# Performance work log

Hardware: AMD Instinct MI355X
Metric: run time of the kernel (lower is better)

Reference implementation:

```python
import jax, jax.numpy as jnp
import numpy as np


def setup_inputs() -> dict:
    key = jax.random.key(0)
    k1, k2, k3 = jax.random.split(key, 3)
    shape = (2, 16, 2048, 64)  # (b, num_heads, seq_len, d_k)
    Q = jax.random.normal(k1, shape, dtype=jnp.float32)
    K = jax.random.normal(k2, shape, dtype=jnp.float32)
    V = jax.random.normal(k3, shape, dtype=jnp.float32)
    return {"Q": Q, "K": K, "V": V}


def reference(Q, K, V):
    # Mathematically identical to the blockwise online-softmax loop:
    # causal softmax attention with scale 1/sqrt(d_k), plus logsumexp L.
    d_k = Q.shape[-1]
    seq_len = Q.shape[2]
    scale = 1.0 / np.sqrt(d_k).astype(np.float32)
    # scores: [b, h, q, k]
    S = jnp.einsum("bhqd,bhkd->bhqk", Q, K) * scale
    causal_mask = jnp.tril(jnp.ones((seq_len, seq_len), dtype=bool))  # k_pos <= q_pos
    S = jnp.where(causal_mask, S, -jnp.inf)
    # L_i = m_i + log(l_i) == logsumexp over key dim (every row has >=1 valid key)
    L = jax.nn.logsumexp(S, axis=-1, keepdims=True)  # [b, h, q, 1]
    P = jnp.exp(S - L)  # normalized probabilities (deferred-normalization result)
    O = jnp.einsum("bhqk,bhkd->bhqd", P, V)
    return O, L
```

## Files before the change

kernel.cpp:

```cpp
#include <hip/hip_runtime.h>
#include <hip/hip_bf16.h>

#define S_LEN 2048
#define DH    64
#define NBH   32
#define KSCALE 0.1803368801111f
#define LN2    0.6931471805599453f
#define MB2    4.0f

typedef short v4s __attribute__((ext_vector_type(4)));
typedef short v8s __attribute__((ext_vector_type(8)));
typedef float v4f __attribute__((ext_vector_type(4)));

__device__ __forceinline__ unsigned short f2bf(float f){
  union { float f; unsigned int u; } v; v.f = f;
  return (unsigned short)((v.u + 0x7FFFu + ((v.u >> 16) & 1u)) >> 16);
}

__device__ __forceinline__ void gld16(void* lds, const void* g){
  __builtin_amdgcn_global_load_lds(
      (const __attribute__((address_space(1))) unsigned int*)g,
      (__attribute__((address_space(3))) unsigned int*)lds, 16, 0, 0);
}

__global__ __launch_bounds__(256) void prep(const float* __restrict__ K,
                                            const float* __restrict__ V,
                                            unsigned short* __restrict__ Kf,
                                            unsigned short* __restrict__ Vf){
  __shared__ unsigned short s[64 * 72];
  const int t   = blockIdx.x;
  const int bh  = blockIdx.y;
  const int tid = threadIdx.x;

  const float* Ksrc = K + ((size_t)bh * S_LEN + t * 64) * DH;
  #pragma unroll
  for (int i = 0; i < 4; ++i){
    int f = tid + i * 256;
    float4 v = ((const float4*)Ksrc)[f];
    int row = f >> 4, col = (f & 15) * 4;
    ushort4 o; o.x = f2bf(v.x); o.y = f2bf(v.y); o.z = f2bf(v.z); o.w = f2bf(v.w);
    *(ushort4*)(&s[row * 72 + col]) = o;
  }
  __syncthreads();
  unsigned short* KfT = Kf + ((size_t)bh * 32 + t) * 4096;
  #pragma unroll
  for (int i = 0; i < 2; ++i){
    int item = tid + i * 256;
    int c = item >> 6, l = item & 63;
    int kb = c >> 1, h = c & 1;
    v8s frag = *(const v8s*)(&s[(kb * 16 + (l & 15)) * 72 + h * 32 + (l >> 4) * 8]);
    *(v8s*)(&KfT[c * 512 + l * 8]) = frag;
  }
  __syncthreads();

  const float* Vsrc = V + ((size_t)bh * S_LEN + t * 64) * DH;
  #pragma unroll
  for (int i = 0; i < 4; ++i){
    int f = tid + i * 256;
    float4 v = ((const float4*)Vsrc)[f];
    int k = f >> 4, d = (f & 15) * 4;
    s[(d + 0) * 72 + k] = f2bf(v.x);
    s[(d + 1) * 72 + k] = f2bf(v.y);
    s[(d + 2) * 72 + k] = f2bf(v.z);
    s[(d + 3) * 72 + k] = f2bf(v.w);
  }
  __syncthreads();
  unsigned short* VfT = Vf + ((size_t)bh * 32 + t) * 4096;
  #pragma unroll
  for (int i = 0; i < 2; ++i){
    int item = tid + i * 256;
    int c = item >> 6, l = item & 63;
    int kb = c >> 1, dp = c & 1;
    int kk = kb * 16 + (l >> 4) * 4;
    v4s a = *(const v4s*)(&s[((dp * 2 + 0) * 16 + (l & 15)) * 72 + kk]);
    v4s b = *(const v4s*)(&s[((dp * 2 + 1) * 16 + (l & 15)) * 72 + kk]);
    v8s fr; fr[0]=a[0]; fr[1]=a[1]; fr[2]=a[2]; fr[3]=a[3];
            fr[4]=b[0]; fr[5]=b[1]; fr[6]=b[2]; fr[7]=b[3];
    *(v8s*)(&VfT[c * 512 + l * 8]) = fr;
  }
}

__global__ __launch_bounds__(512, 8) void fa_fwd(
    const float* __restrict__ Q,
    const unsigned short* __restrict__ Kf,
    const unsigned short* __restrict__ Vf,
    float* __restrict__ O, float* __restrict__ L)
{
  __shared__ __align__(16) char smem[2][16384];

  const int tid  = threadIdx.x;
  const int w    = tid >> 6;
  const int lane = tid & 63;
  const int lq   = lane & 15;
  const int g    = lane >> 4;
  const int kq   = w >> 2;
  const int qs   = w & 3;
  const int bid  = blockIdx.x;
  const int o    = bid >> 5;
  const int hi   = o >> 3, lo = o & 7;
  const int qt   = hi * 8 + ((hi & 1) ? (7 - lo) : lo);
  const int bh   = bid & 31;
  const int M    = qt + 1;

  const unsigned short* KfB = Kf + (size_t)bh * 32 * 4096;
  const unsigned short* VfB = Vf + (size_t)bh * 32 * 4096;

  auto issue = [&](int t, char* buf){
    gld16(buf +        tid * 16, KfB + (size_t)t * 4096 + tid * 8);
    gld16(buf + 8192 + tid * 16, VfB + (size_t)t * 4096 + tid * 8);
  };

  v8s qf[2];
  {
    const float* qp = Q + (size_t)(bh * S_LEN + qt * 64 + qs * 16 + lq) * DH + g * 8;
    #pragma unroll
    for (int h = 0; h < 2; ++h){
      float4 a = *(const float4*)(qp + h * 32);
      float4 b = *(const float4*)(qp + h * 32 + 4);
      v8s qv;
      qv[0]=(short)f2bf(a.x*KSCALE); qv[1]=(short)f2bf(a.y*KSCALE);
      qv[2]=(short)f2bf(a.z*KSCALE); qv[3]=(short)f2bf(a.w*KSCALE);
      qv[4]=(short)f2bf(b.x*KSCALE); qv[5]=(short)f2bf(b.y*KSCALE);
      qv[6]=(short)f2bf(b.z*KSCALE); qv[7]=(short)f2bf(b.w*KSCALE);
      qf[h] = qv;
    }
  }

  issue(0, smem[0]);

  const v4f zero  = {0.f, 0.f, 0.f, 0.f};
  const v4f minit = {-MB2, -MB2, -MB2, -MB2};
  v4f acc[4];
  acc[0] = zero; acc[1] = zero; acc[2] = zero; acc[3] = zero;
  float l1 = 0.f;

  const int kb0 = kq * 2, kb1 = kq * 2 + 1;
  const bool diagLive = (kq * 32 <= qs * 16 + 15);

  for (int t = 0; t < M; ++t){
    const int tn = (t + 1 < M) ? t + 1 : t;
    issue(tn, smem[(t + 1) & 1]);
    asm volatile("s_waitcnt vmcnt(2)" ::: "memory");
    __builtin_amdgcn_s_barrier();
    __builtin_amdgcn_sched_barrier(0);

    if (t < qt || diagLive){
      const char* kbase = smem[t & 1];
      const char* vbase = smem[t & 1] + 8192;

      float p4[2][4];
      __builtin_amdgcn_s_setprio(1);
      #pragma unroll
      for (int j = 0; j < 2; ++j){
        const int kb = kq * 2 + j;
        v8s kf0 = *(const v8s*)(kbase + (kb * 2    ) * 1024 + lane * 16);
        v8s kf1 = *(const v8s*)(kbase + (kb * 2 + 1) * 1024 + lane * 16);
        v4f st = minit;
        st = __builtin_amdgcn_mfma_f32_16x16x32_bf16(kf0, qf[0], st, 0, 0, 0);
        st = __builtin_amdgcn_mfma_f32_16x16x32_bf16(kf1, qf[1], st, 0, 0, 0);
        p4[j][0] = st[0]; p4[j][1] = st[1]; p4[j][2] = st[2]; p4[j][3] = st[3];
      }
      __builtin_amdgcn_s_setprio(0);

      if (t == qt){
        #pragma unroll
        for (int j = 0; j < 2; ++j)
          #pragma unroll
          for (int r = 0; r < 4; ++r)
            if (kq * 32 + j * 16 + g * 4 + r > qs * 16 + lq) p4[j][r] = -INFINITY;
      }

      v4s pf[2];
      #pragma unroll
      for (int j = 0; j < 2; ++j){
        #pragma unroll
        for (int r = 0; r < 4; ++r){
          const float pe = __builtin_amdgcn_exp2f(p4[j][r]);
          p4[j][r] = pe;
          l1 += pe;
        }
        unsigned u0, u1;
        asm("v_cvt_pk_bf16_f32 %0, %1, %2" : "=v"(u0) : "v"(p4[j][0]), "v"(p4[j][1]));
        asm("v_cvt_pk_bf16_f32 %0, %1, %2" : "=v"(u1) : "v"(p4[j][2]), "v"(p4[j][3]));
        union { unsigned u[2]; v4s s4; } P; P.u[0] = u0; P.u[1] = u1;
        pf[j] = P.s4;
      }

      __builtin_amdgcn_s_setprio(1);
      #pragma unroll
      for (int j = 0; j < 2; ++j){
        const int kb = kq * 2 + j;
        #pragma unroll
        for (int dp = 0; dp < 2; ++dp){
          v8s vv8 = *(const v8s*)(vbase + (kb * 2 + dp) * 1024 + lane * 16);
          v4s va0 = {vv8[0], vv8[1], vv8[2], vv8[3]};
          v4s va1 = {vv8[4], vv8[5], vv8[6], vv8[7]};
          acc[dp * 2    ] = __builtin_amdgcn_mfma_f32_16x16x16bf16_1k(va0, pf[j], acc[dp * 2    ], 0, 0, 0);
          acc[dp * 2 + 1] = __builtin_amdgcn_mfma_f32_16x16x16bf16_1k(va1, pf[j], acc[dp * 2 + 1], 0, 0, 0);
        }
      }
      __builtin_amdgcn_s_setprio(0);
    }
    __builtin_amdgcn_s_barrier();
    __builtin_amdgcn_sched_barrier(0);
  }

  asm volatile("s_waitcnt vmcnt(0)" ::: "memory");
  __builtin_amdgcn_sched_barrier(0);
  __syncthreads();

  l1 += __shfl_xor(l1, 16);
  l1 += __shfl_xor(l1, 32);

  float* Lx = (float*)(smem[1]);
  v4f*  Ox = (v4f*)(smem[0]);
  if (kq == 1){
    if (lane < 16) Lx[qs * 16 + lane] = l1;
    #pragma unroll
    for (int db = 0; db < 4; ++db)
      Ox[(qs * 4 + db) * 64 + lane] = acc[db];
  }
  __syncthreads();
  if (kq == 0){
    const float lt   = l1 + Lx[qs * 16 + lq];
    const float invl = 1.f / lt;
    float* Ob = O + ((size_t)bh * S_LEN + qt * 64 + qs * 16 + lq) * DH;
    #pragma unroll
    for (int db = 0; db < 4; ++db){
      v4f o2 = (acc[db] + Ox[(qs * 4 + db) * 64 + lane]) * invl;
      *(v4f*)(Ob + db * 16 + g * 4) = o2;
    }
    if (lane < 16)
      L[(size_t)bh * S_LEN + qt * 64 + qs * 16 + lane] = logf(lt) + MB2 * LN2;
  }
}

__global__ __launch_bounds__(64) void fa_naive(
    const float* __restrict__ Q, const float* __restrict__ K,
    const float* __restrict__ V, float* __restrict__ O, float* __restrict__ L)
{
  const int q  = blockIdx.x;
  const int bh = blockIdx.y;
  const int d  = threadIdx.x;
  const float qv = Q[(size_t)(bh * S_LEN + q) * DH + d];
  float m = -INFINITY, l = 0.f, o = 0.f;
  for (int k = 0; k <= q; ++k){
    float s = qv * K[(size_t)(bh * S_LEN + k) * DH + d];
    #pragma unroll
    for (int off = 32; off > 0; off >>= 1) s += __shfl_xor(s, off);
    s *= 0.125f;
    const float mn = fmaxf(m, s);
    const float sfc = expf(m - mn);
    const float pe = expf(s - mn);
    l = l * sfc + pe;
    o = o * sfc + pe * V[(size_t)(bh * S_LEN + k) * DH + d];
    m = mn;
  }
  O[(size_t)(bh * S_LEN + q) * DH + d] = o / l;
  if (d == 0) L[(size_t)bh * S_LEN + q] = m + logf(l);
}

extern "C" void kernel_launch(void* const* d_in, const int* in_sizes, int n_in,
                              void* d_out, int out_size, void* d_ws, size_t ws_size,
                              hipStream_t stream)
{
  (void)in_sizes; (void)n_in; (void)out_size;
  const float* Q = (const float*)d_in[0];
  const float* K = (const float*)d_in[1];
  const float* V = (const float*)d_in[2];
  float* O = (float*)d_out;
  float* L = O + (size_t)NBH * S_LEN * DH;

  const size_t half = (size_t)NBH * S_LEN * DH * sizeof(unsigned short);
  if (ws_size >= 2 * half){
    unsigned short* Kf = (unsigned short*)d_ws;
    unsigned short* Vf = Kf + (size_t)NBH * S_LEN * DH;
    prep<<<dim3(S_LEN / 64, NBH), 256, 0, stream>>>(K, V, Kf, Vf);
    fa_fwd<<<dim3(1024), 512, 0, stream>>>(Q, Kf, Vf, O, L);
  } else {
    fa_naive<<<dim3(S_LEN, NBH), 64, 0, stream>>>(Q, K, V, O, L);
  }
}
```

Baseline: 43.82 us.

## Process 128-key tiles per iteration to halve barrier-bound loop trips

Each iteration now stages two 64-key K/V tiles (32KB per buffer) and each key-split wave group handles 64 keys instead of 32. This halves the number of loop iterations, barriers and wait points per query tile. The block-to-tile ordering also changes to a four-band snake for load balance. In exchange LDS use doubles and occupancy drops from 8 to 4 blocks per CU, and masking waste on the final tile grows.

```diff
diff --git a/kernel.cpp b/kernel.cpp
--- a/kernel.cpp
+++ b/kernel.cpp
@@ -80,13 +80,13 @@
   }
 }
 
-__global__ __launch_bounds__(512, 8) void fa_fwd(
+__global__ __launch_bounds__(512, 4) void fa_fwd(
     const float* __restrict__ Q,
     const unsigned short* __restrict__ Kf,
     const unsigned short* __restrict__ Vf,
     float* __restrict__ O, float* __restrict__ L)
 {
-  __shared__ __align__(16) char smem[2][16384];
+  __shared__ __align__(16) char smem[2][32768];
 
   const int tid  = threadIdx.x;
   const int w    = tid >> 6;
@@ -97,31 +97,36 @@
   const int qs   = w & 3;
   const int bid  = blockIdx.x;
   const int o    = bid >> 5;
-  const int hi   = o >> 3, lo = o & 7;
-  const int qt   = hi * 8 + ((hi & 1) ? (7 - lo) : lo);
+  const int r4   = o >> 3, a = o & 7;
+  const int qt   = (r4 == 0) ? 31 - a : (r4 == 1) ? 16 + a
+                 : (r4 == 2) ? 15 - a : a;
   const int bh   = bid & 31;
-  const int M    = qt + 1;
+  const int M2   = (qt >> 1) + 1;
+  const int qw0  = qt * 64 + qs * 16;
 
   const unsigned short* KfB = Kf + (size_t)bh * 32 * 4096;
   const unsigned short* VfB = Vf + (size_t)bh * 32 * 4096;
 
   auto issue = [&](int t, char* buf){
-    gld16(buf +        tid * 16, KfB + (size_t)t * 4096 + tid * 8);
-    gld16(buf + 8192 + tid * 16, VfB + (size_t)t * 4096 + tid * 8);
+    const size_t base = (size_t)(2 * t) * 4096;
+    gld16(buf +         tid * 16, KfB + base +        tid * 8);
+    gld16(buf +  8192 + tid * 16, KfB + base + 4096 + tid * 8);
+    gld16(buf + 16384 + tid * 16, VfB + base +        tid * 8);
+    gld16(buf + 24576 + tid * 16, VfB + base + 4096 + tid * 8);
   };
 
   v8s qf[2];
   {
-    const float* qp = Q + (size_t)(bh * S_LEN + qt * 64 + qs * 16 + lq) * DH + g * 8;
+    const float* qp = Q + (size_t)(bh * S_LEN + qw0 + lq) * DH + g * 8;
     #pragma unroll
     for (int h = 0; h < 2; ++h){
-      float4 a = *(const float4*)(qp + h * 32);
-      float4 b = *(const float4*)(qp + h * 32 + 4);
+      float4 aa = *(const float4*)(qp + h * 32);
+      float4 bb = *(const float4*)(qp + h * 32 + 4);
       v8s qv;
-      qv[0]=(short)f2bf(a.x*KSCALE); qv[1]=(short)f2bf(a.y*KSCALE);
-      qv[2]=(short)f2bf(a.z*KSCALE); qv[3]=(short)f2bf(a.w*KSCALE);
-      qv[4]=(short)f2bf(b.x*KSCALE); qv[5]=(short)f2bf(b.y*KSCALE);
-      qv[6]=(short)f2bf(b.z*KSCALE); qv[7]=(short)f2bf(b.w*KSCALE);
+      qv[0]=(short)f2bf(aa.x*KSCALE); qv[1]=(short)f2bf(aa.y*KSCALE);
+      qv[2]=(short)f2bf(aa.z*KSCALE); qv[3]=(short)f2bf(aa.w*KSCALE);
+      qv[4]=(short)f2bf(bb.x*KSCALE); qv[5]=(short)f2bf(bb.y*KSCALE);
+      qv[6]=(short)f2bf(bb.z*KSCALE); qv[7]=(short)f2bf(bb.w*KSCALE);
       qf[h] = qv;
     }
   }
@@ -134,27 +139,27 @@
   acc[0] = zero; acc[1] = zero; acc[2] = zero; acc[3] = zero;
   float l1 = 0.f;
 
-  const int kb0 = kq * 2, kb1 = kq * 2 + 1;
-  const bool diagLive = (kq * 32 <= qs * 16 + 15);
-
-  for (int t = 0; t < M; ++t){
-    const int tn = (t + 1 < M) ? t + 1 : t;
+  for (int t = 0; t < M2; ++t){
+    const int tn = (t + 1 < M2) ? t + 1 : t;
     issue(tn, smem[(t + 1) & 1]);
-    asm volatile("s_waitcnt vmcnt(2)" ::: "memory");
+    asm volatile("s_waitcnt vmcnt(4)" ::: "memory");
     __builtin_amdgcn_s_barrier();
     __builtin_amdgcn_sched_barrier(0);
 
-    if (t < qt || diagLive){
-      const char* kbase = smem[t & 1];
-      const char* vbase = smem[t & 1] + 8192;
-
-      float p4[2][4];
+    const int  kstart = t * 128 + kq * 64;
+    const bool lastT  = (t + 1 == M2);
+    const bool live   = !lastT || (kstart <= qw0 + 15);
+
+    if (live){
+      const char* kbase = smem[t & 1] +         kq * 8192;
+      const char* vbase = smem[t & 1] + 16384 + kq * 8192;
+
+      float p4[4][4];
       __builtin_amdgcn_s_setprio(1);
       #pragma unroll
-      for (int j = 0; j < 2; ++j){
-        const int kb = kq * 2 + j;
-        v8s kf0 = *(const v8s*)(kbase + (kb * 2    ) * 1024 + lane * 16);
-        v8s kf1 = *(const v8s*)(kbase + (kb * 2 + 1) * 1024 + lane * 16);
+      for (int j = 0; j < 4; ++j){
+        v8s kf0 = *(const v8s*)(kbase + (j * 2    ) * 1024 + lane * 16);
+        v8s kf1 = *(const v8s*)(kbase + (j * 2 + 1) * 1024 + lane * 16);
         v4f st = minit;
         st = __builtin_amdgcn_mfma_f32_16x16x32_bf16(kf0, qf[0], st, 0, 0, 0);
         st = __builtin_amdgcn_mfma_f32_16x16x32_bf16(kf1, qf[1], st, 0, 0, 0);
@@ -162,17 +167,17 @@
       }
       __builtin_amdgcn_s_setprio(0);
 
-      if (t == qt){
+      if (lastT){
         #pragma unroll
-        for (int j = 0; j < 2; ++j)
+        for (int j = 0; j < 4; ++j)
           #pragma unroll
           for (int r = 0; r < 4; ++r)
-            if (kq * 32 + j * 16 + g * 4 + r > qs * 16 + lq) p4[j][r] = -INFINITY;
-      }
-
-      v4s pf[2];
+            if (kstart + j * 16 + g * 4 + r > qw0 + lq) p4[j][r] = -INFINITY;
+      }
+
+      v4s pf[4];
       #pragma unroll
-      for (int j = 0; j < 2; ++j){
+      for (int j = 0; j < 4; ++j){
         #pragma unroll
         for (int r = 0; r < 4; ++r){
           const float pe = __builtin_amdgcn_exp2f(p4[j][r]);
@@ -188,11 +193,10 @@
 
       __builtin_amdgcn_s_setprio(1);
       #pragma unroll
-      for (int j = 0; j < 2; ++j){
-        const int kb = kq * 2 + j;
+      for (int j = 0; j < 4; ++j){
         #pragma unroll
         for (int dp = 0; dp < 2; ++dp){
-          v8s vv8 = *(const v8s*)(vbase + (kb * 2 + dp) * 1024 + lane * 16);
+          v8s vv8 = *(const v8s*)(vbase + (j * 2 + dp) * 1024 + lane * 16);
           v4s va0 = {vv8[0], vv8[1], vv8[2], vv8[3]};
           v4s va1 = {vv8[4], vv8[5], vv8[6], vv8[7]};
           acc[dp * 2    ] = __builtin_amdgcn_mfma_f32_16x16x16bf16_1k(va0, pf[j], acc[dp * 2    ], 0, 0, 0);
@@ -224,14 +228,14 @@
   if (kq == 0){
     const float lt   = l1 + Lx[qs * 16 + lq];
     const float invl = 1.f / lt;
-    float* Ob = O + ((size_t)bh * S_LEN + qt * 64 + qs * 16 + lq) * DH;
+    float* Ob = O + ((size_t)bh * S_LEN + qw0 + lq) * DH;
     #pragma unroll
     for (int db = 0; db < 4; ++db){
       v4f o2 = (acc[db] + Ox[(qs * 4 + db) * 64 + lane]) * invl;
       *(v4f*)(Ob + db * 16 + g * 4) = o2;
     }
     if (lane < 16)
-      L[(size_t)bh * S_LEN + qt * 64 + qs * 16 + lane] = logf(lt) + MB2 * LN2;
+      L[(size_t)bh * S_LEN + qw0 + lane] = logf(lt) + MB2 * LN2;
   }
 }
 
```

Result: no change. 44.00 us (+0.4%).
